# Performance work log

Measured on AMD Instinct MI355X. Metric: run time of the kernel, lower is better.

## Reference

```python
import jax, jax.numpy as jnp
import numpy as np
import math

B, N, Q, K = 1, 64, 512, 512
C_Q = C_K = C_V = 256
C_HIDDEN = 32
NO_HEADS = 8
HID = C_HIDDEN * NO_HEADS  # 256


def setup_inputs() -> dict:
    key = jax.random.key(0)
    ks = jax.random.split(key, 12)
    inp = {
        "q_x": jax.random.normal(ks[0], (B, N, Q, C_Q), jnp.float32),
        "k_x": jax.random.normal(ks[1], (B, N, K, C_K), jnp.float32),
        "v_x": jax.random.normal(ks[2], (B, N, K, C_V), jnp.float32),
        "bias_mask": jax.random.normal(ks[3], (B, N, 1, 1, K), jnp.float32),
        "bias_pair": jax.random.normal(ks[4], (B, 1, NO_HEADS, Q, K), jnp.float32),
        # projection weights stored [in, out] (torch Linear is [out, in])
        "wq": jax.random.normal(ks[5], (C_Q, HID), jnp.float32) / math.sqrt(C_Q),
        "wk": jax.random.normal(ks[6], (C_K, HID), jnp.float32) / math.sqrt(C_K),
        "wv": jax.random.normal(ks[7], (C_V, HID), jnp.float32) / math.sqrt(C_V),
        # gating: init weights=0, bias=1 in the module; use small random for a non-trivial test
        "wg": jax.random.normal(ks[8], (C_Q, HID), jnp.float32) * 0.02,
        "bg": jnp.ones((HID,), jnp.float32),
        # output: init 'final' (zeros); use small random for a non-trivial test
        "wo": jax.random.normal(ks[9], (HID, C_Q), jnp.float32) * 0.02,
        "bo": jnp.zeros((C_Q,), jnp.float32),
    }
    return inp


def reference(q_x, k_x, v_x, bias_mask, bias_pair, wq, wk, wv, wg, bg, wo, bo):
    h, c = NO_HEADS, C_HIDDEN
    # projections -> [B, N, Q/K, H, C_h]
    q = (q_x @ wq).reshape(*q_x.shape[:-1], h, c) / math.sqrt(c)
    k = (k_x @ wk).reshape(*k_x.shape[:-1], h, c)
    v = (v_x @ wv).reshape(*v_x.shape[:-1], h, c)
    # logits [B, N, H, Q, K] with additive biases
    a = jnp.einsum("bnqhc,bnkhc->bnhqk", q, k) + bias_mask + bias_pair
    a = jax.nn.softmax(a, axis=-1)
    # output [B, N, Q, H, C_h]
    o = jnp.einsum("bnhqk,bnkhc->bnqhc", a, v)
    # gating
    g = jax.nn.sigmoid((q_x @ wg + bg).reshape(*q_x.shape[:-1], h, c))
    o = o * g
    o = o.reshape(*o.shape[:-2], h * c)
    return o @ wo + bo
```

## Files before the change

kernel.cpp:

```cpp
#include <hip/hip_runtime.h>
#include <math.h>

#define NSEQ   64
#define QLEN   512
#define KLEN   512
#define CIN    256
#define HEADS  8
#define CH     32
#define HIDDIM 256
#define M_TOTAL (NSEQ * QLEN)
#define L2E    1.4426950408889634f

typedef _Float16 f16x8 __attribute__((ext_vector_type(8)));
typedef _Float16 f16x4 __attribute__((ext_vector_type(4)));
typedef __fp16   fp16x2 __attribute__((ext_vector_type(2)));
typedef float    f32x4 __attribute__((ext_vector_type(4)));

__device__ __forceinline__ void gload16(const void* g, void* l) {
    __builtin_amdgcn_global_load_lds(
        (const __attribute__((address_space(1))) void*)g,
        (__attribute__((address_space(3))) void*)l, 16, 0, 0);
}

__device__ __forceinline__ float exp2_fast(float x) {
#if __has_builtin(__builtin_amdgcn_exp2f)
    return __builtin_amdgcn_exp2f(x);
#else
    float r; asm("v_exp_f32 %0, %1" : "=v"(r) : "v"(x)); return r;
#endif
}

__global__ __launch_bounds__(256) void wcast_kernel(
    const float* __restrict__ w0, const float* __restrict__ w1,
    const float* __restrict__ w2, const float* __restrict__ w3,
    const float* __restrict__ w4, _Float16* __restrict__ wt)
{
    __shared__ float t[64][65];
    const float* W;
    switch (blockIdx.z) {
        case 0: W = w0; break; case 1: W = w1; break;
        case 2: W = w2; break; case 3: W = w3; break;
        default: W = w4;
    }
    _Float16* WT = wt + (size_t)blockIdx.z * 65536;
    const int i0 = blockIdx.x * 64, o0 = blockIdx.y * 64;
    const int tid = threadIdx.x;
    const int rr = tid >> 4, c4 = tid & 15;
    #pragma unroll
    for (int i = 0; i < 4; ++i) {
        const int row = rr + i * 16;
        *(float4*)&t[row][c4 * 4] = *(const float4*)&W[(size_t)(i0 + row) * 256 + o0 + c4 * 4];
    }
    __syncthreads();
    #pragma unroll
    for (int i = 0; i < 4; ++i) {
        const int row = rr + i * 16;
        f16x4 v;
        #pragma unroll
        for (int j = 0; j < 4; ++j) v[j] = (_Float16)t[c4 * 4 + j][row];
        *(f16x4*)&WT[(size_t)(o0 + row) * 256 + i0 + c4 * 4] = v;
    }
}

__global__ __launch_bounds__(256) void bpfrag_kernel(
    const float* __restrict__ bias_pair, float* __restrict__ frag)
{
    __shared__ float t[64][68];
    const int qb = blockIdx.x, kb = blockIdx.y, h = blockIdx.z;
    const int tid = threadIdx.x;
    #pragma unroll
    for (int i = 0; i < 4; ++i) {
        const int idx = tid + i * 256;
        const int r = idx >> 4, c4 = idx & 15;
        *(float4*)&t[r][c4 * 4] = *(const float4*)
            &bias_pair[((size_t)h * QLEN + qb * 64 + r) * KLEN + kb * 64 + c4 * 4];
    }
    __syncthreads();
    const int lane = tid & 63, w = tid >> 6;
    const int l15 = lane & 15, quad = lane >> 4;
    const int qt = qb * 4 + w;
    #pragma unroll
    for (int kt2 = 0; kt2 < 4; ++kt2) {
        const int kt = kb * 4 + kt2;
        float4 v;
        v.x = (t[w * 16 + l15][kt2 * 16 + quad * 4 + 0] - 4.0f) * L2E;
        v.y = (t[w * 16 + l15][kt2 * 16 + quad * 4 + 1] - 4.0f) * L2E;
        v.z = (t[w * 16 + l15][kt2 * 16 + quad * 4 + 2] - 4.0f) * L2E;
        v.w = (t[w * 16 + l15][kt2 * 16 + quad * 4 + 3] - 4.0f) * L2E;
        *(float4*)&frag[(((size_t)(h * 32 + qt) * 32) + kt) * 256 + lane * 4] = v;
    }
}

__global__ __launch_bounds__(256) void bmscale_kernel(
    const float* __restrict__ bm, float* __restrict__ o)
{
    const int i = blockIdx.x * 256 + threadIdx.x;
    float4 v = *(const float4*)(bm + (size_t)i * 4);
    v.x *= L2E; v.y *= L2E; v.z *= L2E; v.w *= L2E;
    *(float4*)(o + (size_t)i * 4) = v;
}

__global__ __launch_bounds__(256, 2) void proj_gemm_kernel(
    const float* __restrict__ q_x, const float* __restrict__ k_x,
    const float* __restrict__ v_x, const _Float16* __restrict__ wT,
    const float* __restrict__ bg,
    _Float16* __restrict__ oq, _Float16* __restrict__ ok,
    _Float16* __restrict__ ovT, _Float16* __restrict__ og)
{
    __shared__ __attribute__((aligned(16))) float A_s[2][32 * 256];

    const int combo = blockIdx.x >> 6;
    const int blk   = blockIdx.x & 63;
    const int mode  = combo >> 1;
    const int nhalf = combo & 1;
    const float* A = (mode <= 1) ? q_x : (mode == 2) ? k_x : v_x;
    const _Float16* BT = wT + (size_t)mode * 65536;

    const int tid  = threadIdx.x;
    const int lane = tid & 63, w = tid >> 6;
    const int l15  = lane & 15, quad = lane >> 4;
    const int nw   = nhalf * 128 + w * 32;

    f16x8 bfr[2][8];
    #pragma unroll
    for (int nt = 0; nt < 2; ++nt)
        #pragma unroll
        for (int ks = 0; ks < 8; ++ks)
            bfr[nt][ks] = *(const f16x8*)(BT +
                (size_t)(nw + nt * 16 + l15) * 256 + ks * 32 + quad * 8);

    float bgv[2] = {0.f, 0.f};
    if (mode == 1) { bgv[0] = bg[nw + l15]; bgv[1] = bg[nw + 16 + l15]; }

    const int row_base = blk * 512;

    f32x4 acc[2][2];
    #pragma unroll
    for (int mt = 0; mt < 2; ++mt)
        #pragma unroll
        for (int nt = 0; nt < 2; ++nt) acc[mt][nt] = (f32x4){0.f, 0.f, 0.f, 0.f};

    auto stage = [&](int panel, int buf) {
        const int row0 = row_base + panel * 32;
        #pragma unroll
        for (int j = 0; j < 8; ++j) {
            const int p = tid + j * 256;
            const int r = p >> 6, c = p & 63;
            const int cl = (c & ~7) | ((c & 7) ^ (r & 7));
            gload16(A + (size_t)(row0 + r) * 256 + cl * 4, &A_s[buf][p * 4]);
        }
    };

    stage(0, 0);
    __syncthreads();

    for (int i = 0; i < 16; ++i) {
        if (i < 15) stage(i + 1, (i + 1) & 1);
        const int buf = i & 1;

        #pragma unroll
        for (int ks = 0; ks < 8; ++ks) {
            f16x8 af[2];
            #pragma unroll
            for (int mt = 0; mt < 2; ++mt) {
                const int r  = mt * 16 + l15;
                const int x0 = ks * 8 + ((quad * 2 + 0) ^ (r & 7));
                const int x1 = ks * 8 + ((quad * 2 + 1) ^ (r & 7));
                const f32x4 a0 = *(const f32x4*)&A_s[buf][(r * 64 + x0) * 4];
                const f32x4 a1 = *(const f32x4*)&A_s[buf][(r * 64 + x1) * 4];
                f16x8 v;
                v[0] = (_Float16)a0[0]; v[1] = (_Float16)a0[1];
                v[2] = (_Float16)a0[2]; v[3] = (_Float16)a0[3];
                v[4] = (_Float16)a1[0]; v[5] = (_Float16)a1[1];
                v[6] = (_Float16)a1[2]; v[7] = (_Float16)a1[3];
                af[mt] = v;
            }
            #pragma unroll
            for (int mt = 0; mt < 2; ++mt)
                #pragma unroll
                for (int nt = 0; nt < 2; ++nt)
                    acc[mt][nt] = __builtin_amdgcn_mfma_f32_16x16x32_f16(
                        af[mt], bfr[nt][ks], acc[mt][nt], 0, 0, 0);
        }

        const int row0 = row_base + i * 32;
        if (mode == 3) {
            #pragma unroll
            for (int mt = 0; mt < 2; ++mt) {
                #pragma unroll
                for (int nt = 0; nt < 2; ++nt) {
                    const int col  = nw + nt * 16 + l15;
                    const int rowg = row0 + mt * 16 + quad * 4;
                    const int nn = rowg >> 9, kpos = rowg & 511;
                    f16x4 st;
                    #pragma unroll
                    for (int reg = 0; reg < 4; ++reg) st[reg] = (_Float16)acc[mt][nt][reg];
                    *(f16x4*)&ovT[((size_t)(nn * 256 + col)) * 512 + kpos] = st;
                }
            }
        } else {
            _Float16* C = (mode == 0) ? oq : (mode == 1) ? og : ok;
            #pragma unroll
            for (int mt = 0; mt < 2; ++mt) {
                #pragma unroll
                for (int nt = 0; nt < 2; ++nt) {
                    const int col  = nw + nt * 16 + l15;
                    const int rowg = row0 + mt * 16 + quad * 4;
                    #pragma unroll
                    for (int reg = 0; reg < 4; ++reg) {
                        float x = acc[mt][nt][reg];
                        if (mode == 0) x *= 0.2550348614f;
                        if (mode == 1) { x += bgv[nt]; x = 1.0f / (1.0f + __expf(-x)); }
                        C[(size_t)(rowg + reg) * HIDDIM + col] = (_Float16)x;
                    }
                }
            }
        }
        #pragma unroll
        for (int mt = 0; mt < 2; ++mt)
            #pragma unroll
            for (int nt = 0; nt < 2; ++nt) acc[mt][nt] = (f32x4){0.f, 0.f, 0.f, 0.f};

        __syncthreads();
    }
}

__global__ __launch_bounds__(256, 2) void outproj_kernel(
    const _Float16* __restrict__ Ain, const _Float16* __restrict__ BT,
    const float* __restrict__ bias, float* __restrict__ Cout)
{
    __shared__ __attribute__((aligned(16))) _Float16 A_s[2][32 * 256];

    const int blk   = blockIdx.x & 255;
    const int nhalf = blockIdx.x >> 8;
    const int tid  = threadIdx.x;
    const int lane = tid & 63, w = tid >> 6;
    const int l15  = lane & 15, quad = lane >> 4;
    const int nw   = nhalf * 128 + w * 32;

    f16x8 bfr[2][8];
    #pragma unroll
    for (int nt = 0; nt < 2; ++nt)
        #pragma unroll
        for (int ks = 0; ks < 8; ++ks)
            bfr[nt][ks] = *(const f16x8*)(BT +
                (size_t)(nw + nt * 16 + l15) * 256 + ks * 32 + quad * 8);

    const float bv[2] = { bias[nw + l15], bias[nw + 16 + l15] };
    const int row_base = blk * 128;

    f32x4 acc[2][2];
    #pragma unroll
    for (int mt = 0; mt < 2; ++mt)
        #pragma unroll
        for (int nt = 0; nt < 2; ++nt) acc[mt][nt] = (f32x4){0.f, 0.f, 0.f, 0.f};

    auto stage = [&](int panel, int buf) {
        const int row0 = row_base + panel * 32;
        #pragma unroll
        for (int j = 0; j < 4; ++j) {
            const int p = tid + j * 256;
            const int r = p >> 5, c = p & 31;
            const int cl = (c & ~7) | ((c & 7) ^ (r & 7));
            gload16(Ain + (size_t)(row0 + r) * 256 + cl * 8, &A_s[buf][p * 8]);
        }
    };

    stage(0, 0);
    __syncthreads();

    for (int i = 0; i < 4; ++i) {
        if (i < 3) stage(i + 1, (i + 1) & 1);
        const int buf = i & 1;

        #pragma unroll
        for (int ks = 0; ks < 8; ++ks) {
            f16x8 af[2];
            #pragma unroll
            for (int mt = 0; mt < 2; ++mt) {
                const int r = mt * 16 + l15;
                const int c = (ks * 4 + quad) ^ (r & 7);
                af[mt] = *(const f16x8*)&A_s[buf][r * 256 + c * 8];
            }
            #pragma unroll
            for (int mt = 0; mt < 2; ++mt)
                #pragma unroll
                for (int nt = 0; nt < 2; ++nt)
                    acc[mt][nt] = __builtin_amdgcn_mfma_f32_16x16x32_f16(
                        af[mt], bfr[nt][ks], acc[mt][nt], 0, 0, 0);
        }

        const int row0 = row_base + i * 32;
        #pragma unroll
        for (int mt = 0; mt < 2; ++mt) {
            #pragma unroll
            for (int nt = 0; nt < 2; ++nt) {
                const int col  = nw + nt * 16 + l15;
                const int rowg = row0 + mt * 16 + quad * 4;
                #pragma unroll
                for (int reg = 0; reg < 4; ++reg)
                    Cout[(size_t)(rowg + reg) * HIDDIM + col] = acc[mt][nt][reg] + bv[nt];
            }
        }
        #pragma unroll
        for (int mt = 0; mt < 2; ++mt)
            #pragma unroll
            for (int nt = 0; nt < 2; ++nt) acc[mt][nt] = (f32x4){0.f, 0.f, 0.f, 0.f};

        __syncthreads();
    }
}

__global__ __launch_bounds__(256, 4) void attn_kernel(
    const _Float16* __restrict__ qb, const _Float16* __restrict__ kb,
    const _Float16* __restrict__ vT, const _Float16* __restrict__ gb,
    _Float16* __restrict__ ob,
    const float* __restrict__ bm2, const float* __restrict__ bp_frag)
{
    __shared__ _Float16 k_s[128][40];
    __shared__ _Float16 v_s[32][136];

    const int n    = blockIdx.x;
    const int h    = blockIdx.y;
    const int q0   = blockIdx.z * 128;
    const int tid  = threadIdx.x;
    const int lane = tid & 63;
    const int wq   = tid >> 6;
    const int l15  = lane & 15;
    const int quad = lane >> 4;

    f16x8 qf[2];
    #pragma unroll
    for (int qt = 0; qt < 2; ++qt)
        qf[qt] = *(const f16x8*)(qb +
            (size_t)(n * QLEN + q0 + wq * 32 + qt * 16 + l15) * HIDDIM + h * CH + quad * 8);

    const float* bpf = bp_frag +
        ((size_t)(h * 32 + blockIdx.z * 8 + wq * 2) * 32) * 256 + lane * 4;
    const float* bmb = bm2 + n * KLEN + quad * 4;

    f32x4 o_acc[2][2];
    float l_lane[2] = {0.f, 0.f};
    #pragma unroll
    for (int qt = 0; qt < 2; ++qt)
        #pragma unroll
        for (int ct = 0; ct < 2; ++ct) o_acc[qt][ct] = (f32x4){0.f, 0.f, 0.f, 0.f};

    for (int ch = 0; ch < 4; ++ch) {
        __syncthreads();
        #pragma unroll
        for (int i = 0; i < 2; ++i) {
            const int idx = tid + i * 256;
            const int r = idx >> 2, c8 = idx & 3;
            *(uint4*)&k_s[r][c8 * 8] = *(const uint4*)
                (kb + (size_t)(n * KLEN + ch * 128 + r) * HIDDIM + h * CH + c8 * 8);
            const int vr = idx >> 4, vs = idx & 15;
            *(uint4*)&v_s[vr][vs * 8] = *(const uint4*)
                (vT + ((size_t)(n * HEADS + h) * CH + vr) * KLEN + ch * 128 + vs * 8);
        }
        __syncthreads();

        #pragma unroll
        for (int kt = 0; kt < 8; ++kt) {
            const int kti = ch * 8 + kt;
            const f16x8 kf = *(const f16x8*)&k_s[kt * 16 + l15][quad * 8];
            const float4 bm  = *(const float4*)(bmb + ch * 128 + kt * 16);
            const float4 bp0 = *(const float4*)(bpf + (size_t)kti * 256);
            const float4 bp1 = *(const float4*)(bpf + (size_t)(32 + kti) * 256);
            f32x4 c0, c1;
            c0[0] = bm.x + bp0.x; c0[1] = bm.y + bp0.y;
            c0[2] = bm.z + bp0.z; c0[3] = bm.w + bp0.w;
            c1[0] = bm.x + bp1.x; c1[1] = bm.y + bp1.y;
            c1[2] = bm.z + bp1.z; c1[3] = bm.w + bp1.w;
            __builtin_amdgcn_s_setprio(1);
            const f32x4 s0 = __builtin_amdgcn_mfma_f32_16x16x32_f16(kf, qf[0], c0, 0, 0, 0);
            const f32x4 s1 = __builtin_amdgcn_mfma_f32_16x16x32_f16(kf, qf[1], c1, 0, 0, 0);
            __builtin_amdgcn_s_setprio(0);
            const f16x4 bv0 = *(const f16x4*)&v_s[l15][kt * 16 + quad * 4];
            const f16x4 bv1 = *(const f16x4*)&v_s[16 + l15][kt * 16 + quad * 4];
            #pragma unroll
            for (int qt = 0; qt < 2; ++qt) {
                const f32x4 s = qt ? s1 : s0;
                const float p0 = exp2_fast(s[0]);
                const float p1 = exp2_fast(s[1]);
                const float p2 = exp2_fast(s[2]);
                const float p3 = exp2_fast(s[3]);
                l_lane[qt] += (p0 + p1) + (p2 + p3);
                union { f16x4 v; fp16x2 h[2]; } u;
                u.h[0] = __builtin_amdgcn_cvt_pkrtz(p0, p1);
                u.h[1] = __builtin_amdgcn_cvt_pkrtz(p2, p3);
                __builtin_amdgcn_s_setprio(1);
                o_acc[qt][0] = __builtin_amdgcn_mfma_f32_16x16x16f16(u.v, bv0, o_acc[qt][0], 0, 0, 0);
                o_acc[qt][1] = __builtin_amdgcn_mfma_f32_16x16x16f16(u.v, bv1, o_acc[qt][1], 0, 0, 0);
                __builtin_amdgcn_s_setprio(0);
            }
        }
    }

    float invl[2][4];
    #pragma unroll
    for (int qt = 0; qt < 2; ++qt) {
        float lf = l_lane[qt];
        lf += __shfl_xor(lf, 16);
        lf += __shfl_xor(lf, 32);
        #pragma unroll
        for (int reg = 0; reg < 4; ++reg)
            invl[qt][reg] = 1.0f / __shfl(lf, quad * 4 + reg);
    }

    #pragma unroll
    for (int qt = 0; qt < 2; ++qt) {
        #pragma unroll
        for (int ct = 0; ct < 2; ++ct) {
            #pragma unroll
            for (int reg = 0; reg < 4; ++reg) {
                const int row = q0 + wq * 32 + qt * 16 + quad * 4 + reg;
                const size_t idx = (size_t)(n * QLEN + row) * HIDDIM + h * CH + ct * 16 + l15;
                const float g = (float)gb[idx];
                ob[idx] = (_Float16)(o_acc[qt][ct][reg] * invl[qt][reg] * g);
            }
        }
    }
}

extern "C" void kernel_launch(void* const* d_in, const int* in_sizes, int n_in,
                              void* d_out, int out_size, void* d_ws, size_t ws_size,
                              hipStream_t stream)
{
    const float* q_x       = (const float*)d_in[0];
    const float* k_x       = (const float*)d_in[1];
    const float* v_x       = (const float*)d_in[2];
    const float* bias_mask = (const float*)d_in[3];
    const float* bias_pair = (const float*)d_in[4];
    const float* wq        = (const float*)d_in[5];
    const float* wk        = (const float*)d_in[6];
    const float* wv        = (const float*)d_in[7];
    const float* wg        = (const float*)d_in[8];
    const float* bg        = (const float*)d_in[9];
    const float* wo        = (const float*)d_in[10];
    const float* bo        = (const float*)d_in[11];
    float* out = (float*)d_out;

    const size_t BUF = (size_t)M_TOTAL * HIDDIM;
    _Float16* ws_q  = (_Float16*)d_ws;
    _Float16* ws_k  = ws_q + BUF;
    _Float16* ws_vT = ws_k + BUF;
    _Float16* ws_g  = ws_vT + BUF;
    _Float16* ws_o  = ws_g + BUF;
    _Float16* wT    = ws_o + BUF;
    float*    bpf   = (float*)(wT + 5 * 65536);
    float*    bm2   = bpf + (size_t)8 * 512 * 512;

    wcast_kernel<<<dim3(4, 4, 5), 256, 0, stream>>>(wq, wg, wk, wv, wo, wT);
    bpfrag_kernel<<<dim3(8, 8, 8), 256, 0, stream>>>(bias_pair, bpf);
    bmscale_kernel<<<dim3(32), 256, 0, stream>>>(bias_mask, bm2);

    proj_gemm_kernel<<<dim3(512), 256, 0, stream>>>(
        q_x, k_x, v_x, wT, bg, ws_q, ws_k, ws_vT, ws_g);

    attn_kernel<<<dim3(NSEQ, HEADS, QLEN / 128), 256, 0, stream>>>(
        ws_q, ws_k, ws_vT, ws_g, ws_o, bm2, bpf);

    outproj_kernel<<<dim3(512), 256, 0, stream>>>(
        ws_o, wT + 4 * 65536, bo, out);
}
```

Measured before the change: 252.8 us.

## Stage projection input as fp16 in LDS via register prefetch, raise occupancy

The projection GEMM now loads each fp32 input panel into registers, converts it to fp16 once, and writes it to LDS with an XOR swizzle. This replaces the direct global-to-LDS fp32 copies that were re-read and re-converted inside the MFMA loop. Halving LDS per block lets launch bounds go from 2 to 3 blocks per CU, and fragment reads become a single 16-byte load. The trade-off is that the global loads now pass through registers, which raises register pressure and exposes load latency before the LDS write at the end of each iteration.

```diff
diff --git a/kernel.cpp b/kernel.cpp
--- a/kernel.cpp
+++ b/kernel.cpp
@@ -100,14 +100,14 @@
     *(float4*)(o + (size_t)i * 4) = v;
 }
 
-__global__ __launch_bounds__(256, 2) void proj_gemm_kernel(
+__global__ __launch_bounds__(256, 3) void proj_gemm_kernel(
     const float* __restrict__ q_x, const float* __restrict__ k_x,
     const float* __restrict__ v_x, const _Float16* __restrict__ wT,
     const float* __restrict__ bg,
     _Float16* __restrict__ oq, _Float16* __restrict__ ok,
     _Float16* __restrict__ ovT, _Float16* __restrict__ og)
 {
-    __shared__ __attribute__((aligned(16))) float A_s[2][32 * 256];
+    __shared__ __attribute__((aligned(16))) _Float16 A_s[2][32 * 256];
 
     const int combo = blockIdx.x >> 6;
     const int blk   = blockIdx.x & 63;
@@ -140,23 +140,42 @@
         #pragma unroll
         for (int nt = 0; nt < 2; ++nt) acc[mt][nt] = (f32x4){0.f, 0.f, 0.f, 0.f};
 
-    auto stage = [&](int panel, int buf) {
+    float4 sreg[8];
+
+    auto gload_panel = [&](int panel) {
         const int row0 = row_base + panel * 32;
         #pragma unroll
-        for (int j = 0; j < 8; ++j) {
+        for (int j = 0; j < 4; ++j) {
             const int p = tid + j * 256;
-            const int r = p >> 6, c = p & 63;
-            const int cl = (c & ~7) | ((c & 7) ^ (r & 7));
-            gload16(A + (size_t)(row0 + r) * 256 + cl * 4, &A_s[buf][p * 4]);
+            const int r = p >> 5, c = p & 31;
+            const float* ap = A + (size_t)(row0 + r) * 256 + c * 8;
+            sreg[j * 2]     = *(const float4*)ap;
+            sreg[j * 2 + 1] = *(const float4*)(ap + 4);
         }
     };
 
-    stage(0, 0);
+    auto swrite_panel = [&](int buf) {
+        #pragma unroll
+        for (int j = 0; j < 4; ++j) {
+            const int p = tid + j * 256;
+            const int r = p >> 5, c = p & 31;
+            const int cp = c ^ (r & 15);
+            f16x8 v;
+            v[0] = (_Float16)sreg[j * 2].x;     v[1] = (_Float16)sreg[j * 2].y;
+            v[2] = (_Float16)sreg[j * 2].z;     v[3] = (_Float16)sreg[j * 2].w;
+            v[4] = (_Float16)sreg[j * 2 + 1].x; v[5] = (_Float16)sreg[j * 2 + 1].y;
+            v[6] = (_Float16)sreg[j * 2 + 1].z; v[7] = (_Float16)sreg[j * 2 + 1].w;
+            *(f16x8*)&A_s[buf][(r * 32 + cp) * 8] = v;
+        }
+    };
+
+    gload_panel(0);
+    swrite_panel(0);
     __syncthreads();
 
     for (int i = 0; i < 16; ++i) {
-        if (i < 15) stage(i + 1, (i + 1) & 1);
         const int buf = i & 1;
+        if (i < 15) gload_panel(i + 1);
 
         #pragma unroll
         for (int ks = 0; ks < 8; ++ks) {
@@ -164,16 +183,8 @@
             #pragma unroll
             for (int mt = 0; mt < 2; ++mt) {
                 const int r  = mt * 16 + l15;
-                const int x0 = ks * 8 + ((quad * 2 + 0) ^ (r & 7));
-                const int x1 = ks * 8 + ((quad * 2 + 1) ^ (r & 7));
-                const f32x4 a0 = *(const f32x4*)&A_s[buf][(r * 64 + x0) * 4];
-                const f32x4 a1 = *(const f32x4*)&A_s[buf][(r * 64 + x1) * 4];
-                f16x8 v;
-                v[0] = (_Float16)a0[0]; v[1] = (_Float16)a0[1];
-                v[2] = (_Float16)a0[2]; v[3] = (_Float16)a0[3];
-                v[4] = (_Float16)a1[0]; v[5] = (_Float16)a1[1];
-                v[6] = (_Float16)a1[2]; v[7] = (_Float16)a1[3];
-                af[mt] = v;
+                const int cp = (ks * 4 + quad) ^ (r & 15);
+                af[mt] = *(const f16x8*)&A_s[buf][(r * 32 + cp) * 8];
             }
             #pragma unroll
             for (int mt = 0; mt < 2; ++mt)
@@ -221,6 +232,7 @@
             #pragma unroll
             for (int nt = 0; nt < 2; ++nt) acc[mt][nt] = (f32x4){0.f, 0.f, 0.f, 0.f};
 
+        if (i < 15) swrite_panel(buf ^ 1);
         __syncthreads();
     }
 }
```

Result: no change. 257.6 us (+1.9%).
